# Kernel tuning notes

Hardware: AMD Instinct MI355X
Metric: run time of the kernel (lower is better)

Reference implementation:

```python
import jax, jax.numpy as jnp
import numpy as np
import math

B, T = 256, 512
NUM_PANEL, STATIC, TIME_DIM, HID = 27, 6, 10, 128
MAX_LEN = 1500


def _gru(x, Wih, Whh, bih, bhh):
    # x: [S, N, D]; scan over S. Torch GRU gate order: r, z, n.
    H = Whh.shape[1]
    gi = jnp.einsum('snd,gd->sng', x, Wih) + bih  # [S, N, 3H] input projections
    def step(h, gi_t):
        gh = h @ Whh.T + bhh
        i_r, i_z, i_n = jnp.split(gi_t, 3, axis=-1)
        h_r, h_z, h_n = jnp.split(gh, 3, axis=-1)
        r = jax.nn.sigmoid(i_r + h_r)
        z = jax.nn.sigmoid(i_z + h_z)
        n = jnp.tanh(i_n + r * h_n)
        h2 = (1.0 - z) * n + z * h
        return h2, h2
    h0 = jnp.zeros((x.shape[1], H), x.dtype)
    _, hs = jax.lax.scan(step, h0, gi)
    return hs  # [S, N, H]


def _prefix_attn(h, w, b):
    # GRU_Attention loop: for each t, softmax over prefix scores e[:, :t+1]
    # and context c_t = sum_j alpha_j * h_j. GRU is causal so prefix rerun
    # equals full-run prefix; fold the loop into one masked triangular softmax.
    e = jnp.einsum('bth,h->bt', h, w[0]) + b[0]            # [B, T]
    Tl = h.shape[1]
    mask = jnp.tril(jnp.ones((Tl, Tl), bool))              # [T, T], j <= t
    scores = jnp.where(mask[None], e[:, None, :], -1e30)   # [B, T, T]
    A = jax.nn.softmax(scores, axis=-1)
    return jnp.einsum('btj,bjh->bth', A, h)                # [B, T, H]


def _make_params(key):
    ks = iter(jax.random.split(key, 32))
    def lin(shape, scale):
        return (jax.random.normal(next(ks), shape, jnp.float32) * scale)
    d_sh = 2 * NUM_PANEL + STATIC + TIME_DIM          # 70
    d_t1 = HID + NUM_PANEL + 1 + STATIC + TIME_DIM    # 172
    d_t2 = HID + NUM_PANEL + 1 + NUM_PANEL + STATIC + TIME_DIM  # 199
    p = {}
    p['rte_W'] = lin((TIME_DIM, TIME_DIM), 1.0 / math.sqrt(TIME_DIM))
    p['rte_b'] = jnp.zeros((TIME_DIM,), jnp.float32)
    for tag, d in (('sh', d_sh), ('t1', d_t1), ('t2', d_t2)):
        s = 1.0 / math.sqrt(HID)
        p[tag + '_Wih'] = lin((3 * HID, d), s)
        p[tag + '_Whh'] = lin((3 * HID, HID), s)
        p[tag + '_bih'] = jnp.zeros((3 * HID,), jnp.float32)
        p[tag + '_bhh'] = jnp.zeros((3 * HID,), jnp.float32)
    for tag in ('t1', 't2'):
        p[tag + '_w'] = lin((1, HID), 1.0 / math.sqrt(HID))
        p[tag + '_wb'] = jnp.zeros((1,), jnp.float32)
    return p


def _rte_table():
    pos = np.arange(MAX_LEN, dtype=np.float32)[:, None]
    div = np.exp(np.arange(0, TIME_DIM, 2, dtype=np.float32) * (-math.log(10000.0) / TIME_DIM))
    emb = np.zeros((MAX_LEN, TIME_DIM), np.float32)
    emb[:, 0::2] = np.sin(pos * div) / math.sqrt(TIME_DIM)
    emb[:, 1::2] = np.cos(pos * div) / math.sqrt(TIME_DIM)
    return jnp.asarray(emb)


def setup_inputs() -> dict:
    key = jax.random.key(0)
    k1, k2, k3, k4, k5, kp = jax.random.split(key, 6)
    inp = {
        'input_batch': jax.random.normal(k1, (B, T, NUM_PANEL), jnp.float32),
        'hgb_delta': jax.random.normal(k2, (B, T, 1), jnp.float32),
        'static_feature': jax.random.normal(k3, (B, T, STATIC), jnp.float32),
        'nnan_mask': jax.random.uniform(k4, (B, T, NUM_PANEL), jnp.float32),
        'test_time_delta': jax.random.randint(k5, (B, T, 1), 0, MAX_LEN, jnp.int32),
        'rte_emb': _rte_table(),
    }
    inp.update(_make_params(kp))
    return inp


def reference(input_batch, hgb_delta, static_feature, nnan_mask, rte_emb,
              rte_W, rte_b,
              sh_Wih, sh_Whh, sh_bih, sh_bhh,
              t1_Wih, t1_Whh, t1_bih, t1_bhh, t1_w, t1_wb,
              t2_Wih, t2_Whh, t2_bih, t2_bhh, t2_w, t2_wb,
              test_time_delta):
    # RelTemporalEncoding: frozen sinusoidal embedding lookup + Linear
    tt = rte_emb[test_time_delta[..., 0]] @ rte_W.T + rte_b  # [B, T, time_dim]
    x_sh = jnp.concatenate([input_batch, nnan_mask, static_feature, tt], -1)
    # shared nn.GRU has batch_first=False but receives [B, T, F]:
    # faithfully recur over axis 0 (B) with batch axis T.
    h_sh = _gru(x_sh, sh_Wih, sh_Whh, sh_bih, sh_bhh)  # [B, T, HID]
    x1 = jnp.concatenate([h_sh, nnan_mask, hgb_delta, static_feature, tt], -1)
    x2 = jnp.concatenate([h_sh, nnan_mask, hgb_delta, input_batch, static_feature, tt], -1)
    # task GRUs are batch_first=True: recur over time
    h1 = jnp.swapaxes(_gru(jnp.swapaxes(x1, 0, 1), t1_Wih, t1_Whh, t1_bih, t1_bhh), 0, 1)
    h2 = jnp.swapaxes(_gru(jnp.swapaxes(x2, 0, 1), t2_Wih, t2_Whh, t2_bih, t2_bhh), 0, 1)
    c1 = _prefix_attn(h1, t1_w, t1_wb)  # [B, T, HID]
    c2 = _prefix_attn(h2, t2_w, t2_wb)
    return (c1, c2)


if __name__ == '__main__':
    out = reference(**setup_inputs())
    print(out[0].shape, out[1].shape)
```

## Files before the change

### kernel.cpp

```cpp
#include <hip/hip_runtime.h>
#include <stdint.h>

typedef unsigned int uint;
typedef unsigned short ushort;
typedef unsigned long long u64;

#define BATCH 256
#define TLEN  512
#define BT    (BATCH*TLEN)
#define HID   128
#define G3    384


struct Tab { const void* p[24]; int sz[24]; };

typedef __attribute__((ext_vector_type(8))) short bf16x8;
typedef __attribute__((ext_vector_type(4))) float f32x4;

__device__ __forceinline__ float b2f(ushort u) { return __uint_as_float(((uint)u) << 16); }
__device__ __forceinline__ ushort f2b(float f) {
  uint x = __float_as_uint(f);
  return (ushort)((x + 0x7fffu + ((x >> 16) & 1u)) >> 16);
}
__device__ __forceinline__ float loadf(const void* p, int i, int bf) {
  return bf ? b2f(((const ushort*)p)[i]) : ((const float*)p)[i];
}
__device__ __forceinline__ float sanz(float x) { return fminf(1e4f, fmaxf(-1e4f, x)); }

__device__ __forceinline__ float sigmoidf_(float x) { return 1.0f / (1.0f + __expf(-x)); }
__device__ __forceinline__ float tanhf_(float x) {
  x = fminf(10.0f, fmaxf(-10.0f, x));
  float t = __expf(-2.0f * x);
  return __fdividef(1.0f - t, 1.0f + t);
}

__device__ __forceinline__ float dot2(uint w, uint v, float acc) {
  acc = fmaf(__uint_as_float(w << 16), __uint_as_float(v << 16), acc);
  acc = fmaf(__uint_as_float(w & 0xffff0000u), __uint_as_float(v & 0xffff0000u), acc);
  return acc;
}
__device__ __forceinline__ void dot2x4(uint4 w, uint4 v, float& a0, float& a1) {
  a0 = dot2(w.x, v.x, a0);
  a1 = dot2(w.y, v.y, a1);
  a0 = dot2(w.z, v.z, a0);
  a1 = dot2(w.w, v.w, a1);
}
__device__ __forceinline__ float blo(uint u)  { return __uint_as_float(u << 16); }
__device__ __forceinline__ float bhi_(uint u) { return __uint_as_float(u & 0xffff0000u); }

__device__ bool emb_ok_dev(const void* q, int bfc) {
  if (q == nullptr) return false;
  if (bfc) {
    const ushort* us = (const ushort*)q;
    float v1 = b2f(us[1]), v10 = b2f(us[10]), v11 = b2f(us[11]);
    return us[0] == 0 && v1 > 0.30f && v1 < 0.33f && v10 > 0.25f && v10 < 0.28f &&
           v11 > 0.16f && v11 < 0.18f;
  } else {
    const float* f = (const float*)q;
    return f[0] == 0.0f && f[1] > 0.31f && f[1] < 0.322f && f[10] > 0.26f &&
           f[10] < 0.272f && f[11] > 0.165f && f[11] < 0.176f;
  }
}

__global__ void detect_kernel(Tab tab, u64* __restrict__ ptab, int* __restrict__ flags) {
  if (threadIdx.x != 0) return;
  const int elems[24] = {3538944,131072,786432,3538944,131072,15000,100,10,
                         26880,49152,384,384,66048,49152,384,384,
                         76416,49152,384,384,128,1,128,1};
  const int sigm[24] = {0,1,2,3,23,4,5,6,7,8,9,10,11,12,13,14,17,18,19,20,15,16,21,22};
  int map[24];
  int bf = -1;
  bool done = false;
  for (int interp = 0; interp < 3 && !done; interp++) {
    int assigned[24];
    for (int r = 0; r < 24; r++) assigned[r] = 0;
    bool ok = true;
    for (int i = 0; i < 24 && ok; i++) {
      bool found = false;
      for (int r = 0; r < 24; r++) {
        int e = elems[r];
        if (interp == 1) e *= (r == 4) ? 4 : 2;
        if (interp == 2) e *= 4;
        if (!assigned[r] && tab.sz[i] == e) { map[r] = i; assigned[r] = 1; found = true; break; }
      }
      if (!found) ok = false;
    }
    if (!ok) continue;
    int bfc = (interp == 0) ? ((((const ushort*)tab.p[map[5]])[1] != 0) ? 1 : 0)
                            : ((interp == 1) ? 1 : 0);
    if (emb_ok_dev(tab.p[map[5]], bfc)) { bf = bfc; done = true; }
  }
  if (!done) {
    const void* q5 = tab.p[5];
    int b5 = (((const ushort*)q5)[1] != 0) ? 1 : 0;
    if (emb_ok_dev(q5, b5)) {
      for (int r = 0; r < 24; r++) map[r] = r;
      bf = b5; done = true;
    }
  }
  if (!done) {
    const void* q4 = tab.p[4];
    int b4 = (((const ushort*)q4)[1] != 0) ? 1 : 0;
    if (emb_ok_dev(q4, b4)) {
      for (int r = 0; r < 24; r++) map[r] = sigm[r];
      bf = b4; done = true;
    }
  }
  if (!done) {
    for (int r = 0; r < 24; r++) map[r] = r;
    bf = (((const ushort*)tab.p[5])[1] != 0) ? 1 : 0;
  }
  for (int r = 0; r < 24; r++) ptab[r] = (u64)tab.p[map[r]];
  flags[0] = bf;
  const void* tq = tab.p[map[4]];
  const int* ti = (const int*)tq;
  const float* tf = (const float*)tq;
  int ok_i = 1, ok_f = 1;
  for (int k = 0; k < 64; k++) {
    int i = k * 16 + 3;
    int vi = ti[i];
    if (vi < 0 || vi >= 1500) ok_i = 0;
    float vf = tf[i];
    if (!(vf >= 0.f && vf < 1500.f && vf == floorf(vf))) ok_f = 0;
  }
  flags[1] = ok_i ? 0 : (ok_f ? 1 : 2);
}

__global__ void __launch_bounds__(256) tt_kernel(const u64* __restrict__ ptab,
                                                 const int* __restrict__ flags,
                                                 ushort* __restrict__ tt) {
  const int bf = flags[0];
  const int tmode = flags[1];
  const void* ttd = (const void*)ptab[4];
  const void* emb = (const void*)ptab[5];
  const void* W   = (const void*)ptab[6];
  const void* bb  = (const void*)ptab[7];
  int n = blockIdx.x * blockDim.x + threadIdx.x;
  if (n >= BT) return;
  int idx;
  if (tmode == 0)      idx = ((const int*)ttd)[n];
  else if (tmode == 1) idx = (int)((const float*)ttd)[n];
  else                 idx = (int)b2f(((const ushort*)ttd)[n]);
  if (idx < 0) idx = 0;
  if (idx >= 1500) idx = 1499;
  float e[10];
#pragma unroll
  for (int j = 0; j < 10; j++) e[j] = sanz(loadf(emb, idx * 10 + j, bf));
#pragma unroll
  for (int k = 0; k < 10; k++) {
    float acc = sanz(loadf(bb, k, bf));
#pragma unroll
    for (int j = 0; j < 10; j++) acc = fmaf(e[j], sanz(loadf(W, k * 10 + j, bf)), acc);
    tt[n * 10 + k] = f2b(acc);
  }
}

__global__ void __launch_bounds__(256) wpack_kernel(
    const u64* __restrict__ ptab, const int* __restrict__ flags,
    ushort* __restrict__ wp_sh, ushort* __restrict__ wp_t1,
    ushort* __restrict__ wp_t2, float* __restrict__ biasb) {
  const int bf = flags[0];
  const int m = blockIdx.x % 3;
  const int slice = blockIdx.x / 3;
  const int tid = threadIdx.x;
  const void* W  = (const void*)ptab[m == 0 ? 8 : (m == 1 ? 12 : 16)];
  const void* bi = (const void*)ptab[m == 0 ? 10 : (m == 1 ? 14 : 18)];
  const int DIN = m == 0 ? 70 : (m == 1 ? 172 : 199);
  const int KP  = m == 0 ? 96 : (m == 1 ? 192 : 224);
  ushort* dst = m == 0 ? wp_sh : (m == 1 ? wp_t1 : wp_t2);
  const int total = G3 * KP;
  const int per = total / 16;
  const int lo = slice * per, hi = lo + per;
  for (int idx = lo + tid; idx < hi; idx += 256) {
    int r = idx / KP, k = idx - r * KP;
    float v = (k < DIN) ? sanz(loadf(W, r * DIN + k, bf)) : 0.f;
    dst[idx] = f2b(v);
  }
  if (slice == 0) {
    for (int g = tid; g < G3; g += 256) biasb[m * G3 + g] = sanz(loadf(bi, g, bf));
  }
}

template <int MODE>
__global__ void __launch_bounds__(256, 2) gi_mfma_kernel(
    const u64* __restrict__ ptab, const int* __restrict__ flags,
    const ushort* __restrict__ tt, const ushort* __restrict__ hsh,
    const ushort* __restrict__ Wp, const float* __restrict__ biasb,
    void* __restrict__ gout, int gi32) {
  constexpr int DIN = MODE == 0 ? 70 : (MODE == 1 ? 172 : 199);
  constexpr int KP  = MODE == 0 ? 96 : (MODE == 1 ? 192 : 224);
  constexpr int STR = KP + 8;
  __shared__ alignas(16) ushort xs[64 * STR];
  __shared__ alignas(16) float bls[G3];
  (void)DIN;

  const int bf = flags[0];
  const int tid = threadIdx.x;
  const int n0 = blockIdx.x * 64;
  const void* xin  = (const void*)ptab[0];
  const void* hgb  = (const void*)ptab[1];
  const void* stat = (const void*)ptab[2];
  const void* nnan = (const void*)ptab[3];

  for (int g = tid; g < G3; g += 256) bls[g] = biasb[MODE * G3 + g];

  if (MODE == 0) {
    for (int idx = tid; idx < 64 * KP; idx += 256) {
      int r = idx / KP, d = idx - r * KP;
      int n = n0 + r;
      float v = 0.f;
      if (d < 27)       v = loadf(xin, n * 27 + d, bf);
      else if (d < 54)  v = loadf(nnan, n * 27 + (d - 27), bf);
      else if (d < 60)  v = loadf(stat, n * 6 + (d - 54), bf);
      else if (d < 70)  v = b2f(tt[n * 10 + (d - 60)]);
      xs[r * STR + d] = f2b(sanz(v));
    }
  } else {
    for (int idx = tid; idx < 64 * 16; idx += 256) {
      int r = idx >> 4, c = idx & 15;
      uint4 v = ((const uint4*)(hsh + (size_t)(n0 + r) * HID))[c];
      *(uint4*)&xs[r * STR + c * 8] = v;
    }
    constexpr int REM = KP - 128;
    for (int idx = tid; idx < 64 * REM; idx += 256) {
      int r = idx / REM, d = 128 + (idx - r * REM);
      int n = n0 + r;
      float v = 0.f;
      if (d < 155)      v = loadf(nnan, n * 27 + (d - 128), bf);
      else if (d < 156) v = loadf(hgb, n, bf);
      else if (MODE == 2) {
        if (d < 183)      v = loadf(xin, n * 27 + (d - 156), bf);
        else if (d < 189) v = loadf(stat, n * 6 + (d - 183), bf);
        else if (d < 199) v = b2f(tt[n * 10 + (d - 189)]);
      } else {
        if (d < 162)      v = loadf(stat, n * 6 + (d - 156), bf);
        else if (d < 172) v = b2f(tt[n * 10 + (d - 162)]);
      }
      xs[r * STR + d] = f2b(sanz(v));
    }
  }
  __syncthreads();

  const int l  = tid & 63;
  const int wv = tid >> 6;
  const int lr = l & 15;
  const int kg = l >> 4;
  const int g0 = wv * 96;

  f32x4 acc[6][4];
#pragma unroll
  for (int mi = 0; mi < 6; mi++) {
    f32x4 bv = *(const f32x4*)&bls[g0 + mi * 16 + kg * 4];
#pragma unroll
    for (int ni = 0; ni < 4; ni++) acc[mi][ni] = bv;
  }

  const ushort* wbase = Wp + (size_t)(g0 + lr) * KP + kg * 8;
#pragma unroll
  for (int ks = 0; ks < KP; ks += 32) {
    bf16x8 av[6], bvv[4];
#pragma unroll
    for (int mi = 0; mi < 6; mi++)
      av[mi] = *(const bf16x8*)(wbase + (size_t)mi * 16 * KP + ks);
#pragma unroll
    for (int ni = 0; ni < 4; ni++)
      bvv[ni] = *(const bf16x8*)&xs[(ni * 16 + lr) * STR + ks + kg * 8];
#pragma unroll
    for (int mi = 0; mi < 6; mi++)
#pragma unroll
      for (int ni = 0; ni < 4; ni++)
        acc[mi][ni] = __builtin_amdgcn_mfma_f32_16x16x32_bf16(
            av[mi], bvv[ni], acc[mi][ni], 0, 0, 0);
  }

#pragma unroll
  for (int ni = 0; ni < 4; ni++) {
    const size_t nrow = (size_t)(n0 + ni * 16 + lr);
    if (gi32) {
      float* gp = (float*)gout + nrow * G3 + g0 + kg * 4;
#pragma unroll
      for (int mi = 0; mi < 6; mi++) *(f32x4*)(gp + mi * 16) = acc[mi][ni];
    } else {
      ushort* gp = (ushort*)gout + nrow * G3 + g0 + kg * 4;
#pragma unroll
      for (int mi = 0; mi < 6; mi++) {
        uint2 pkt;
        pkt.x = (uint)f2b(acc[mi][ni].x) | ((uint)f2b(acc[mi][ni].y) << 16);
        pkt.y = (uint)f2b(acc[mi][ni].z) | ((uint)f2b(acc[mi][ni].w) << 16);
        *(uint2*)(gp + mi * 16) = pkt;
      }
    }
  }
}

__global__ void __launch_bounds__(384, 3) scan_kernel(
    const u64* __restrict__ ptab, const int* __restrict__ flags,
    const void* __restrict__ gi_0, const void* __restrict__ gi_1, int gi32,
    ushort* __restrict__ out_0, ushort* __restrict__ out_1,
    int whh0, int bhh0, int whh1, int bhh1, int nsteps, int axis) {
  __shared__ alignas(16) float hf[HID];
  __shared__ alignas(16) float Ah[G3];

  const int bf = flags[0];
  const int tid = threadIdx.x;
  const int sel = (axis && blockIdx.x >= BATCH) ? 1 : 0;
  const int lane = axis ? (blockIdx.x & (BATCH - 1)) : blockIdx.x;
  const void* Whh = (const void*)ptab[sel ? whh1 : whh0];
  const void* bhh = (const void*)ptab[sel ? bhh1 : bhh0];
  const void* gi  = sel ? gi_1 : gi_0;
  ushort* hout    = sel ? out_1 : out_0;

  uint4 wh[16];
#pragma unroll
  for (int c = 0; c < 16; c++) {
    uint pk[4];
#pragma unroll
    for (int e = 0; e < 4; e++) {
      int p = c * 4 + e;
      uint lo = (uint)f2b(sanz(loadf(Whh, tid * HID + 2 * p, bf)));
      uint hi = (uint)f2b(sanz(loadf(Whh, tid * HID + 2 * p + 1, bf)));
      pk[e] = lo | (hi << 16);
    }
    wh[c] = make_uint4(pk[0], pk[1], pk[2], pk[3]);
  }
  const float bh = sanz(loadf(bhh, tid, bf));

  if (tid < HID) hf[tid] = 0.f;
  float hprev = 0.f;
  __syncthreads();

#pragma unroll 1
  for (int s = 0; s < nsteps; s++) {
    const int n = axis ? (lane * TLEN + s) : (s * TLEN + lane);
    const size_t base = (size_t)n * G3;
    float gv0 = 0.f, gv1 = 0.f, gv2 = 0.f;
    if (tid < HID) {
      if (gi32) {
        const float* g = (const float*)gi;
        gv0 = g[base + tid]; gv1 = g[base + HID + tid]; gv2 = g[base + 2 * HID + tid];
      } else {
        const ushort* g = (const ushort*)gi;
        gv0 = b2f(g[base + tid]); gv1 = b2f(g[base + HID + tid]); gv2 = b2f(g[base + 2 * HID + tid]);
      }
    }
    float a0 = 0.f, a1 = 0.f;
    const float4* h4 = (const float4*)hf;
#pragma unroll
    for (int c = 0; c < 16; c++) {
      uint4 wv = wh[c];
      float4 x0 = h4[2 * c];
      float4 x1 = h4[2 * c + 1];
      a0 = fmaf(blo(wv.x), x0.x, a0); a1 = fmaf(bhi_(wv.x), x0.y, a1);
      a0 = fmaf(blo(wv.y), x0.z, a0); a1 = fmaf(bhi_(wv.y), x0.w, a1);
      a0 = fmaf(blo(wv.z), x1.x, a0); a1 = fmaf(bhi_(wv.z), x1.y, a1);
      a0 = fmaf(blo(wv.w), x1.z, a0); a1 = fmaf(bhi_(wv.w), x1.w, a1);
    }
    Ah[tid] = a0 + a1 + bh;
    __syncthreads();

    if (tid < HID) {
      float r  = sigmoidf_(gv0 + Ah[tid]);
      float z  = sigmoidf_(gv1 + Ah[HID + tid]);
      float nn = tanhf_(gv2 + r * Ah[2 * HID + tid]);
      float h2 = (1.0f - z) * nn + z * hprev;
      hprev = h2;
      hout[(size_t)n * HID + tid] = f2b(h2);
      hf[tid] = h2;
    }
    __syncthreads();
  }
}

#define SH_DIN  70
#define SH_DINP 72
#define SH_NP4  9

__global__ void __launch_bounds__(G3) shared_gru_kernel(
    const u64* __restrict__ ptab, const int* __restrict__ flags,
    const ushort* __restrict__ tt, ushort* __restrict__ hsh) {
  __shared__ alignas(16) ushort xs[SH_DINP];
  __shared__ alignas(16) ushort hhi[HID];
  __shared__ alignas(16) ushort hlo[HID];
  __shared__ float Ai[G3];
  __shared__ float Ah[G3];

  const int bf = flags[0];
  const void* xin  = (const void*)ptab[0];
  const void* stat = (const void*)ptab[2];
  const void* nnan = (const void*)ptab[3];
  const void* Wih  = (const void*)ptab[8];
  const void* Whh  = (const void*)ptab[9];
  const void* bih  = (const void*)ptab[10];
  const void* bhh  = (const void*)ptab[11];
  const int tid = threadIdx.x;
  const int t = blockIdx.x;

  uint4 wi4[SH_NP4];
#pragma unroll
  for (int c = 0; c < SH_NP4; c++) {
    uint pk[4];
#pragma unroll
    for (int e = 0; e < 4; e++) {
      int p = c * 4 + e;
      uint lo = (2 * p < SH_DIN) ? (uint)f2b(sanz(loadf(Wih, tid * SH_DIN + 2 * p, bf))) : 0u;
      uint hi = (2 * p + 1 < SH_DIN) ? (uint)f2b(sanz(loadf(Wih, tid * SH_DIN + 2 * p + 1, bf))) : 0u;
      pk[e] = lo | (hi << 16);
    }
    wi4[c] = make_uint4(pk[0], pk[1], pk[2], pk[3]);
  }
  uint4 wh4[16];
#pragma unroll
  for (int c = 0; c < 16; c++) {
    uint pk[4];
#pragma unroll
    for (int e = 0; e < 4; e++) {
      int p = c * 4 + e;
      uint lo = (uint)f2b(sanz(loadf(Whh, tid * HID + 2 * p, bf)));
      uint hi = (uint)f2b(sanz(loadf(Whh, tid * HID + 2 * p + 1, bf)));
      pk[e] = lo | (hi << 16);
    }
    wh4[c] = make_uint4(pk[0], pk[1], pk[2], pk[3]);
  }
  const float bi = sanz(loadf(bih, tid, bf));
  const float bh = sanz(loadf(bhh, tid, bf));

  if (tid < HID) { hhi[tid] = 0; hlo[tid] = 0; }
  if (tid >= SH_DIN && tid < SH_DINP) xs[tid] = 0;
  float hprev = 0.0f;
  __syncthreads();

#pragma unroll 1
  for (int b = 0; b < BATCH; b++) {
    const int n = b * TLEN + t;
    if (tid < SH_DIN) {
      float v;
      if (tid < 27)       v = loadf(xin, n * 27 + tid, bf);
      else if (tid < 54)  v = loadf(nnan, n * 27 + (tid - 27), bf);
      else if (tid < 60)  v = loadf(stat, n * 6 + (tid - 54), bf);
      else                v = b2f(tt[n * 10 + (tid - 60)]);
      xs[tid] = f2b(sanz(v));
    }
    __syncthreads();

    float g0 = bi, g1 = 0.0f;
    const uint4* xs4 = (const uint4*)xs;
#pragma unroll
    for (int c = 0; c < SH_NP4; c++) dot2x4(wi4[c], xs4[c], g0, g1);

    float h0 = bh, h1 = 0.0f;
    const uint4* hh4 = (const uint4*)hhi;
    const uint4* hl4 = (const uint4*)hlo;
#pragma unroll
    for (int c = 0; c < 16; c++) {
      dot2x4(wh4[c], hh4[c], h0, h1);
      dot2x4(wh4[c], hl4[c], h0, h1);
    }
    Ai[tid] = g0 + g1;
    Ah[tid] = h0 + h1;
    __syncthreads();

    if (tid < HID) {
      float r = sigmoidf_(Ai[tid] + Ah[tid]);
      float z = sigmoidf_(Ai[HID + tid] + Ah[HID + tid]);
      float nn = tanhf_(Ai[2 * HID + tid] + r * Ah[2 * HID + tid]);
      float h2 = (1.0f - z) * nn + z * hprev;
      hprev = h2;
      hsh[n * HID + tid] = f2b(h2);
      uint hb = __float_as_uint(h2) & 0xffff0000u;
      hhi[tid] = (ushort)(hb >> 16);
      hlo[tid] = f2b(h2 - __uint_as_float(hb));
    }
  }
}

#define T_DINP 200
#define T_NP4  25

__global__ void __launch_bounds__(G3) task_gru_kernel(
    const u64* __restrict__ ptab, const int* __restrict__ flags,
    const ushort* __restrict__ hsh, const ushort* __restrict__ tt,
    ushort* __restrict__ h1o, ushort* __restrict__ h2o) {
  __shared__ alignas(16) ushort xs[T_DINP];
  __shared__ alignas(16) ushort hhi[HID];
  __shared__ alignas(16) ushort hlo[HID];
  __shared__ float Ai[G3];
  __shared__ float Ah[G3];

  const int bf = flags[0];
  const int tid = threadIdx.x;
  const int is2 = (blockIdx.x >= BATCH) ? 1 : 0;
  const int b = blockIdx.x & (BATCH - 1);
  const int DIN = is2 ? 199 : 172;
  const void* xin  = (const void*)ptab[0];
  const void* hgb  = (const void*)ptab[1];
  const void* stat = (const void*)ptab[2];
  const void* nnan = (const void*)ptab[3];
  const void* Wih  = (const void*)ptab[is2 ? 16 : 12];
  const void* Whh  = (const void*)ptab[is2 ? 17 : 13];
  const void* bihp = (const void*)ptab[is2 ? 18 : 14];
  const void* bhhp = (const void*)ptab[is2 ? 19 : 15];
  ushort* hout = is2 ? h2o : h1o;

  uint4 wi4[T_NP4];
#pragma unroll
  for (int c = 0; c < T_NP4; c++) {
    uint pk[4];
#pragma unroll
    for (int e = 0; e < 4; e++) {
      int p = c * 4 + e;
      uint lo = (2 * p < DIN) ? (uint)f2b(sanz(loadf(Wih, tid * DIN + 2 * p, bf))) : 0u;
      uint hi = (2 * p + 1 < DIN) ? (uint)f2b(sanz(loadf(Wih, tid * DIN + 2 * p + 1, bf))) : 0u;
      pk[e] = lo | (hi << 16);
    }
    wi4[c] = make_uint4(pk[0], pk[1], pk[2], pk[3]);
  }
  uint4 wh4[16];
#pragma unroll
  for (int c = 0; c < 16; c++) {
    uint pk[4];
#pragma unroll
    for (int e = 0; e < 4; e++) {
      int p = c * 4 + e;
      uint lo = (uint)f2b(sanz(loadf(Whh, tid * HID + 2 * p, bf)));
      uint hi = (uint)f2b(sanz(loadf(Whh, tid * HID + 2 * p + 1, bf)));
      pk[e] = lo | (hi << 16);
    }
    wh4[c] = make_uint4(pk[0], pk[1], pk[2], pk[3]);
  }
  const float bi = sanz(loadf(bihp, tid, bf));
  const float bh = sanz(loadf(bhhp, tid, bf));

  if (tid < HID) { hhi[tid] = 0; hlo[tid] = 0; }
  if (tid >= DIN && tid < T_DINP) xs[tid] = 0;
  float hprev = 0.0f;
  __syncthreads();

#pragma unroll 1
  for (int t = 0; t < TLEN; t++) {
    const int n = b * TLEN + t;
    if (tid < DIN) {
      float v;
      if (tid < 128)        v = b2f(hsh[n * HID + tid]);
      else if (tid < 155)   v = loadf(nnan, n * 27 + (tid - 128), bf);
      else if (tid < 156)   v = loadf(hgb, n, bf);
      else if (is2) {
        if (tid < 183)      v = loadf(xin, n * 27 + (tid - 156), bf);
        else if (tid < 189) v = loadf(stat, n * 6 + (tid - 183), bf);
        else                v = b2f(tt[n * 10 + (tid - 189)]);
      } else {
        if (tid < 162)      v = loadf(stat, n * 6 + (tid - 156), bf);
        else                v = b2f(tt[n * 10 + (tid - 162)]);
      }
      xs[tid] = f2b(sanz(v));
    }
    __syncthreads();

    float g0 = bi, g1 = 0.0f;
    const uint4* xs4 = (const uint4*)xs;
#pragma unroll
    for (int c = 0; c < T_NP4; c++) dot2x4(wi4[c], xs4[c], g0, g1);

    float h0 = bh, h1 = 0.0f;
    const uint4* hh4 = (const uint4*)hhi;
    const uint4* hl4 = (const uint4*)hlo;
#pragma unroll
    for (int c = 0; c < 16; c++) {
      dot2x4(wh4[c], hh4[c], h0, h1);
      dot2x4(wh4[c], hl4[c], h0, h1);
    }
    Ai[tid] = g0 + g1;
    Ah[tid] = h0 + h1;
    __syncthreads();

    if (tid < HID) {
      float r = sigmoidf_(Ai[tid] + Ah[tid]);
      float z = sigmoidf_(Ai[HID + tid] + Ah[HID + tid]);
      float nn = tanhf_(Ai[2 * HID + tid] + r * Ah[2 * HID + tid]);
      float h2 = (1.0f - z) * nn + z * hprev;
      hprev = h2;
      hout[n * HID + tid] = f2b(h2);
      uint hb = __float_as_uint(h2) & 0xffff0000u;
      hhi[tid] = (ushort)(hb >> 16);
      hlo[tid] = f2b(h2 - __uint_as_float(hb));
    }
  }
}

__global__ void __launch_bounds__(128) attn_kernel(
    const u64* __restrict__ ptab, const int* __restrict__ flags,
    const ushort* __restrict__ h1, const ushort* __restrict__ h2,
    float* __restrict__ outp) {
  __shared__ float pl[TLEN];
  __shared__ alignas(16) uint wp[64];
  __shared__ float red[2];

  const int bf = flags[0];
  const int is2 = (blockIdx.x >= BATCH) ? 1 : 0;
  const int b = blockIdx.x & (BATCH - 1);
  const int tid = threadIdx.x;
  const ushort* h = is2 ? h2 : h1;
  const void* w  = (const void*)ptab[is2 ? 22 : 20];
  const void* wb = (const void*)ptab[is2 ? 23 : 21];
  float* out = outp + (size_t)is2 * BT * HID;

  if (tid < 64) {
    uint lo = (uint)f2b(sanz(loadf(w, 2 * tid, bf)));
    uint hi = (uint)f2b(sanz(loadf(w, 2 * tid + 1, bf)));
    wp[tid] = lo | (hi << 16);
  }
  __syncthreads();
  const float wbf = sanz(loadf(wb, 0, bf));

  float e[4];
  const uint4* wp4 = (const uint4*)wp;
#pragma unroll
  for (int q = 0; q < 4; q++) {
    int j = q * 128 + tid;
    const uint4* hr4 = (const uint4*)(h + (size_t)(b * TLEN + j) * HID);
    float a0 = 0.f, a1 = 0.f;
#pragma unroll
    for (int c = 0; c < 16; c++) {
      uint4 hv = hr4[c];
      uint4 wv = wp4[c];
      a0 = dot2(hv.x, wv.x, a0);
      a1 = dot2(hv.y, wv.y, a1);
      a0 = dot2(hv.z, wv.z, a0);
      a1 = dot2(hv.w, wv.w, a1);
    }
    e[q] = a0 + a1 + wbf;
    pl[j] = e[q];
  }
  float m = fmaxf(fmaxf(e[0], e[1]), fmaxf(e[2], e[3]));
#pragma unroll
  for (int off = 32; off > 0; off >>= 1) m = fmaxf(m, __shfl_down(m, off));
  if ((tid & 63) == 0) red[tid >> 6] = m;
  __syncthreads();
  m = fmaxf(red[0], red[1]);
#pragma unroll
  for (int q = 0; q < 4; q++) {
    int j = q * 128 + tid;
    pl[j] = __expf(pl[j] - m);
  }
  __syncthreads();

  float s = 0.f, acc = 0.f;
  const ushort* hc = h + (size_t)b * TLEN * HID + tid;
  float* oc = out + (size_t)b * TLEN * HID + tid;
#pragma unroll 1
  for (int j = 0; j < TLEN; j++) {
    float pj = pl[j];
    s += pj;
    acc = fmaf(pj, b2f(hc[j * HID]), acc);
    oc[j * HID] = __fdividef(acc, fmaxf(s, 1e-37f));
  }
}

extern "C" void kernel_launch(void* const* d_in, const int* in_sizes, int n_in,
                              void* d_out, int out_size, void* d_ws, size_t ws_size,
                              hipStream_t stream) {
  (void)out_size;
  Tab tab;
  for (int i = 0; i < 24; i++) {
    tab.p[i] = (i < n_in) ? d_in[i] : nullptr;
    tab.sz[i] = (i < n_in) ? in_sizes[i] : -1;
  }

  const size_t WPSH = (size_t)G3 * 96 * 2;
  const size_t WPT1 = (size_t)G3 * 192 * 2;
  const size_t WPT2 = (size_t)G3 * 224 * 2;
  const size_t BIAS = 3 * G3 * 4;
  const size_t packo = 256;
  const size_t datao = packo + WPSH + WPT1 + WPT2 + BIAS;
  const size_t fixed = datao + (size_t)BT * 10 * 2 + 3ull * BT * HID * 2;
  const size_t gif = (size_t)BT * G3 * 4;
  const size_t gib = (size_t)BT * G3 * 2;
  int tier;
  if      (ws_size >= fixed + 2 * gif) tier = 1;
  else if (ws_size >= fixed + gif)     tier = 2;
  else if (ws_size >= fixed + gib)     tier = 3;
  else if (ws_size >= fixed)           tier = 4;
  else return;

  u64* ptab    = (u64*)d_ws;
  int* flags   = (int*)((char*)d_ws + 192);
  ushort* wpsh = (ushort*)((char*)d_ws + packo);
  ushort* wpt1 = (ushort*)((char*)d_ws + packo + WPSH);
  ushort* wpt2 = (ushort*)((char*)d_ws + packo + WPSH + WPT1);
  float* biasb = (float*)((char*)d_ws + packo + WPSH + WPT1 + WPT2);
  ushort* tt   = (ushort*)((char*)d_ws + datao);
  ushort* hsh  = tt + (size_t)BT * 10;
  ushort* h1   = hsh + (size_t)BT * HID;
  ushort* h2   = h1 + (size_t)BT * HID;
  float* out   = (float*)d_out;

  detect_kernel<<<dim3(1), dim3(64), 0, stream>>>(tab, ptab, flags);
  tt_kernel<<<dim3(BT / 256), dim3(256), 0, stream>>>(ptab, flags, tt);

  if (tier == 4) {
    shared_gru_kernel<<<dim3(TLEN), dim3(G3), 0, stream>>>(ptab, flags, tt, hsh);
    task_gru_kernel<<<dim3(2 * BATCH), dim3(G3), 0, stream>>>(ptab, flags, hsh, tt, h1, h2);
    attn_kernel<<<dim3(2 * BATCH), dim3(128), 0, stream>>>(ptab, flags, h1, h2, out);
    return;
  }

  wpack_kernel<<<dim3(48), dim3(256), 0, stream>>>(ptab, flags, wpsh, wpt1, wpt2, biasb);

  const int gi32 = (tier <= 2) ? 1 : 0;
  const size_t esz = gi32 ? 4 : 2;
  char* giA = (char*)d_ws + fixed;
  char* giB = giA + (size_t)BT * G3 * esz;

  gi_mfma_kernel<0><<<dim3(BT / 64), dim3(256), 0, stream>>>(
      ptab, flags, tt, hsh, wpsh, biasb, giA, gi32);
  scan_kernel<<<dim3(TLEN), dim3(G3), 0, stream>>>(ptab, flags, giA, giA, gi32,
                                                   hsh, hsh, 9, 11, 9, 11, BATCH, 0);

  if (tier == 1) {
    gi_mfma_kernel<1><<<dim3(BT / 64), dim3(256), 0, stream>>>(
        ptab, flags, tt, hsh, wpt1, biasb, giB, gi32);
    gi_mfma_kernel<2><<<dim3(BT / 64), dim3(256), 0, stream>>>(
        ptab, flags, tt, hsh, wpt2, biasb, giA, gi32);
    scan_kernel<<<dim3(2 * BATCH), dim3(G3), 0, stream>>>(ptab, flags, giB, giA, gi32,
                                                          h1, h2, 13, 15, 17, 19, TLEN, 1);
  } else {
    gi_mfma_kernel<1><<<dim3(BT / 64), dim3(256), 0, stream>>>(
        ptab, flags, tt, hsh, wpt1, biasb, giA, gi32);
    scan_kernel<<<dim3(BATCH), dim3(G3), 0, stream>>>(ptab, flags, giA, giA, gi32,
                                                      h1, h1, 13, 15, 13, 15, TLEN, 1);
    gi_mfma_kernel<2><<<dim3(BT / 64), dim3(256), 0, stream>>>(
        ptab, flags, tt, hsh, wpt2, biasb, giA, gi32);
    scan_kernel<<<dim3(BATCH), dim3(G3), 0, stream>>>(ptab, flags, giA, giA, gi32,
                                                      h2, h2, 17, 19, 17, 19, TLEN, 1);
  }
  attn_kernel<<<dim3(2 * BATCH), dim3(128), 0, stream>>>(ptab, flags, h1, h2, out);
}
```

Measured before the change: 2.309 ms.

## Batch 16 GRU sequences per block and compute recurrence with bf16 MFMA

Replaces the per-sequence scalar GRU scan (one block per sequence, FMA dot products against register-held weights) with a block that advances 16 sequences together. The hidden-state matvec becomes 16x16x32 bf16 MFMA tiles, with h split into hi/lo bf16 halves to keep near-fp32 accuracy. Next-step input gates are prefetched into registers, and h is double-buffered in LDS so each step needs one barrier instead of two. Trade-off: far fewer blocks (32 for the shared GRU, 16-32 for the task GRUs), which may leave most CUs idle. Each MFMA is also issued twice (hi and lo) on the serial critical path.

```diff
diff --git a/kernel.cpp b/kernel.cpp
--- a/kernel.cpp
+++ b/kernel.cpp
@@ -16,6 +16,7 @@
 
 typedef __attribute__((ext_vector_type(8))) short bf16x8;
 typedef __attribute__((ext_vector_type(4))) float f32x4;
+typedef __attribute__((ext_vector_type(4))) ushort u16x4;
 
 __device__ __forceinline__ float b2f(ushort u) { return __uint_as_float(((uint)u) << 16); }
 __device__ __forceinline__ ushort f2b(float f) {
@@ -45,8 +46,6 @@
   a0 = dot2(w.z, v.z, a0);
   a1 = dot2(w.w, v.w, a1);
 }
-__device__ __forceinline__ float blo(uint u)  { return __uint_as_float(u << 16); }
-__device__ __forceinline__ float bhi_(uint u) { return __uint_as_float(u & 0xffff0000u); }
 
 __device__ bool emb_ok_dev(const void* q, int bfc) {
   if (q == nullptr) return false;
@@ -293,81 +292,155 @@
   }
 }
 
-__global__ void __launch_bounds__(384, 3) scan_kernel(
+__global__ void __launch_bounds__(256, 1) scan_mfma_kernel(
     const u64* __restrict__ ptab, const int* __restrict__ flags,
     const void* __restrict__ gi_0, const void* __restrict__ gi_1, int gi32,
     ushort* __restrict__ out_0, ushort* __restrict__ out_1,
-    int whh0, int bhh0, int whh1, int bhh1, int nsteps, int axis) {
-  __shared__ alignas(16) float hf[HID];
-  __shared__ alignas(16) float Ah[G3];
+    int whh0, int bhh0, int whh1, int bhh1,
+    int nsteps, int axis, int bps) {
+  __shared__ alignas(16) ushort hbuf[2][2][16][136];
 
   const int bf = flags[0];
   const int tid = threadIdx.x;
-  const int sel = (axis && blockIdx.x >= BATCH) ? 1 : 0;
-  const int lane = axis ? (blockIdx.x & (BATCH - 1)) : blockIdx.x;
+  const int sel = (blockIdx.x >= bps) ? 1 : 0;
+  const int sb  = sel ? (blockIdx.x - bps) : blockIdx.x;
+  const int seq0 = sb * 16;
   const void* Whh = (const void*)ptab[sel ? whh1 : whh0];
   const void* bhh = (const void*)ptab[sel ? bhh1 : bhh0];
   const void* gi  = sel ? gi_1 : gi_0;
   ushort* hout    = sel ? out_1 : out_0;
 
-  uint4 wh[16];
-#pragma unroll
-  for (int c = 0; c < 16; c++) {
-    uint pk[4];
-#pragma unroll
-    for (int e = 0; e < 4; e++) {
-      int p = c * 4 + e;
-      uint lo = (uint)f2b(sanz(loadf(Whh, tid * HID + 2 * p, bf)));
-      uint hi = (uint)f2b(sanz(loadf(Whh, tid * HID + 2 * p + 1, bf)));
-      pk[e] = lo | (hi << 16);
-    }
-    wh[c] = make_uint4(pk[0], pk[1], pk[2], pk[3]);
-  }
-  const float bh = sanz(loadf(bhh, tid, bf));
-
-  if (tid < HID) hf[tid] = 0.f;
-  float hprev = 0.f;
+  const int l  = tid & 63;
+  const int wv = tid >> 6;
+  const int lr = l & 15;
+  const int kg = l >> 4;
+
+  int gb[6];
+#pragma unroll
+  for (int c = 0; c < 3; c++) {
+    gb[2 * c]     = c * 128 + 32 * wv;
+    gb[2 * c + 1] = c * 128 + 32 * wv + 16;
+  }
+
+  bf16x8 av[6][4];
+#pragma unroll
+  for (int mt = 0; mt < 6; mt++) {
+    const int grow = gb[mt] + lr;
+#pragma unroll
+    for (int ks = 0; ks < 4; ks++) {
+#pragma unroll
+      for (int j = 0; j < 8; j++)
+        av[mt][ks][j] =
+            (short)f2b(sanz(loadf(Whh, grow * HID + ks * 32 + kg * 8 + j, bf)));
+    }
+  }
+  f32x4 bh4[6];
+#pragma unroll
+  for (int mt = 0; mt < 6; mt++) {
+#pragma unroll
+    for (int j = 0; j < 4; j++)
+      bh4[mt][j] = sanz(loadf(bhh, gb[mt] + kg * 4 + j, bf));
+  }
+
+  for (int i = tid; i < 2 * 16 * 136; i += 256) ((ushort*)hbuf[0])[i] = 0;
+
+  const size_t row0 = axis ? ((size_t)(seq0 + lr) * TLEN) : (size_t)(seq0 + lr);
+  const size_t nstr = axis ? 1 : TLEN;
+  ushort* hp = hout + row0 * HID + 32 * wv + kg * 4;
+
+  f32x4 gp[6];
+  {
+    const size_t nb = row0 * G3;
+    if (gi32) {
+#pragma unroll
+      for (int mt = 0; mt < 6; mt++)
+        gp[mt] = *(const f32x4*)((const float*)gi + nb + gb[mt] + kg * 4);
+    } else {
+#pragma unroll
+      for (int mt = 0; mt < 6; mt++) {
+        uint2 u = *(const uint2*)((const ushort*)gi + nb + gb[mt] + kg * 4);
+        f32x4 v;
+        v.x = b2f((ushort)(u.x & 0xffffu)); v.y = b2f((ushort)(u.x >> 16));
+        v.z = b2f((ushort)(u.y & 0xffffu)); v.w = b2f((ushort)(u.y >> 16));
+        gp[mt] = v;
+      }
+    }
+  }
+
+  f32x4 hprev0, hprev1;
+#pragma unroll
+  for (int j = 0; j < 4; j++) { hprev0[j] = 0.f; hprev1[j] = 0.f; }
+
   __syncthreads();
+  int cur = 0;
 
 #pragma unroll 1
   for (int s = 0; s < nsteps; s++) {
-    const int n = axis ? (lane * TLEN + s) : (s * TLEN + lane);
-    const size_t base = (size_t)n * G3;
-    float gv0 = 0.f, gv1 = 0.f, gv2 = 0.f;
-    if (tid < HID) {
+    f32x4 acc[6];
+#pragma unroll
+    for (int mt = 0; mt < 4; mt++) acc[mt] = gp[mt] + bh4[mt];
+    f32x4 gin0 = gp[4], gin1 = gp[5];
+    acc[4] = bh4[4];
+    acc[5] = bh4[5];
+
+    {
+      const int sn = (s + 1 < nsteps) ? s + 1 : s;
+      const size_t nb = (row0 + (size_t)sn * nstr) * G3;
       if (gi32) {
-        const float* g = (const float*)gi;
-        gv0 = g[base + tid]; gv1 = g[base + HID + tid]; gv2 = g[base + 2 * HID + tid];
+#pragma unroll
+        for (int mt = 0; mt < 6; mt++)
+          gp[mt] = *(const f32x4*)((const float*)gi + nb + gb[mt] + kg * 4);
       } else {
-        const ushort* g = (const ushort*)gi;
-        gv0 = b2f(g[base + tid]); gv1 = b2f(g[base + HID + tid]); gv2 = b2f(g[base + 2 * HID + tid]);
+#pragma unroll
+        for (int mt = 0; mt < 6; mt++) {
+          uint2 u = *(const uint2*)((const ushort*)gi + nb + gb[mt] + kg * 4);
+          f32x4 v;
+          v.x = b2f((ushort)(u.x & 0xffffu)); v.y = b2f((ushort)(u.x >> 16));
+          v.z = b2f((ushort)(u.y & 0xffffu)); v.w = b2f((ushort)(u.y >> 16));
+          gp[mt] = v;
+        }
       }
     }
-    float a0 = 0.f, a1 = 0.f;
-    const float4* h4 = (const float4*)hf;
-#pragma unroll
-    for (int c = 0; c < 16; c++) {
-      uint4 wv = wh[c];
-      float4 x0 = h4[2 * c];
-      float4 x1 = h4[2 * c + 1];
-      a0 = fmaf(blo(wv.x), x0.x, a0); a1 = fmaf(bhi_(wv.x), x0.y, a1);
-      a0 = fmaf(blo(wv.y), x0.z, a0); a1 = fmaf(bhi_(wv.y), x0.w, a1);
-      a0 = fmaf(blo(wv.z), x1.x, a0); a1 = fmaf(bhi_(wv.z), x1.y, a1);
-      a0 = fmaf(blo(wv.w), x1.z, a0); a1 = fmaf(bhi_(wv.w), x1.w, a1);
-    }
-    Ah[tid] = a0 + a1 + bh;
+
+#pragma unroll
+    for (int ks = 0; ks < 4; ks++) {
+      bf16x8 bhi = *(const bf16x8*)&hbuf[cur][0][lr][ks * 32 + kg * 8];
+      bf16x8 blo = *(const bf16x8*)&hbuf[cur][1][lr][ks * 32 + kg * 8];
+#pragma unroll
+      for (int mt = 0; mt < 6; mt++) {
+        acc[mt] = __builtin_amdgcn_mfma_f32_16x16x32_bf16(av[mt][ks], bhi, acc[mt], 0, 0, 0);
+        acc[mt] = __builtin_amdgcn_mfma_f32_16x16x32_bf16(av[mt][ks], blo, acc[mt], 0, 0, 0);
+      }
+    }
+
+#pragma unroll
+    for (int q = 0; q < 2; q++) {
+      f32x4 rr = acc[q], zz = acc[2 + q], np = acc[4 + q];
+      f32x4 gq = q ? gin1 : gin0;
+      f32x4 hpv = q ? hprev1 : hprev0;
+      f32x4 h2;
+      u16x4 hi4, lo4, rt4;
+#pragma unroll
+      for (int j = 0; j < 4; j++) {
+        float r  = sigmoidf_(rr[j]);
+        float z  = sigmoidf_(zz[j]);
+        float nn = tanhf_(gq[j] + r * np[j]);
+        float hv = (1.0f - z) * nn + z * hpv[j];
+        h2[j] = hv;
+        uint hb = __float_as_uint(hv) & 0xffff0000u;
+        hi4[j] = (ushort)(hb >> 16);
+        lo4[j] = f2b(hv - __uint_as_float(hb));
+        rt4[j] = f2b(hv);
+      }
+      if (q) hprev1 = h2; else hprev0 = h2;
+      const int hb0 = 32 * wv + 16 * q + kg * 4;
+      *(u16x4*)&hbuf[cur ^ 1][0][lr][hb0] = hi4;
+      *(u16x4*)&hbuf[cur ^ 1][1][lr][hb0] = lo4;
+      *(u16x4*)(hp + (size_t)s * nstr * HID + 16 * q) = rt4;
+    }
+
     __syncthreads();
-
-    if (tid < HID) {
-      float r  = sigmoidf_(gv0 + Ah[tid]);
-      float z  = sigmoidf_(gv1 + Ah[HID + tid]);
-      float nn = tanhf_(gv2 + r * Ah[2 * HID + tid]);
-      float h2 = (1.0f - z) * nn + z * hprev;
-      hprev = h2;
-      hout[(size_t)n * HID + tid] = f2b(h2);
-      hf[tid] = h2;
-    }
-    __syncthreads();
+    cur ^= 1;
   }
 }
 
@@ -712,25 +785,25 @@
 
   gi_mfma_kernel<0><<<dim3(BT / 64), dim3(256), 0, stream>>>(
       ptab, flags, tt, hsh, wpsh, biasb, giA, gi32);
-  scan_kernel<<<dim3(TLEN), dim3(G3), 0, stream>>>(ptab, flags, giA, giA, gi32,
-                                                   hsh, hsh, 9, 11, 9, 11, BATCH, 0);
+  scan_mfma_kernel<<<dim3(TLEN / 16), dim3(256), 0, stream>>>(
+      ptab, flags, giA, giA, gi32, hsh, hsh, 9, 11, 9, 11, BATCH, 0, TLEN / 16);
 
   if (tier == 1) {
     gi_mfma_kernel<1><<<dim3(BT / 64), dim3(256), 0, stream>>>(
         ptab, flags, tt, hsh, wpt1, biasb, giB, gi32);
     gi_mfma_kernel<2><<<dim3(BT / 64), dim3(256), 0, stream>>>(
         ptab, flags, tt, hsh, wpt2, biasb, giA, gi32);
-    scan_kernel<<<dim3(2 * BATCH), dim3(G3), 0, stream>>>(ptab, flags, giB, giA, gi32,
-                                                          h1, h2, 13, 15, 17, 19, TLEN, 1);
+    scan_mfma_kernel<<<dim3(2 * BATCH / 16), dim3(256), 0, stream>>>(
+        ptab, flags, giB, giA, gi32, h1, h2, 13, 15, 17, 19, TLEN, 1, BATCH / 16);
   } else {
     gi_mfma_kernel<1><<<dim3(BT / 64), dim3(256), 0, stream>>>(
         ptab, flags, tt, hsh, wpt1, biasb, giA, gi32);
-    scan_kernel<<<dim3(BATCH), dim3(G3), 0, stream>>>(ptab, flags, giA, giA, gi32,
-                                                      h1, h1, 13, 15, 13, 15, TLEN, 1);
+    scan_mfma_kernel<<<dim3(BATCH / 16), dim3(256), 0, stream>>>(
+        ptab, flags, giA, giA, gi32, h1, h1, 13, 15, 13, 15, TLEN, 1, BATCH / 16);
     gi_mfma_kernel<2><<<dim3(BT / 64), dim3(256), 0, stream>>>(
         ptab, flags, tt, hsh, wpt2, biasb, giA, gi32);
-    scan_kernel<<<dim3(BATCH), dim3(G3), 0, stream>>>(ptab, flags, giA, giA, gi32,
-                                                      h2, h2, 17, 19, 17, 19, TLEN, 1);
+    scan_mfma_kernel<<<dim3(BATCH / 16), dim3(256), 0, stream>>>(
+        ptab, flags, giA, giA, gi32, h2, h2, 17, 19, 17, 19, TLEN, 1, BATCH / 16);
   }
   attn_kernel<<<dim3(2 * BATCH), dim3(128), 0, stream>>>(ptab, flags, h1, h2, out);
 }
```

Result: faster. 2.198 ms (-4.8%).
